# Kernel tuning notes

Hardware: AMD Instinct MI355X
Metric: run time of the kernel (lower is better)

## Reference

```python
import jax, jax.numpy as jnp
import numpy as np
from jax import lax

N_IN, N_H = 3, 2
N_REC = N_IN + N_H  # 5 qubits in the recurrent cell


def _ry(theta):
    # theta: (B,) -> (B, 2, 2) complex64 RY matrices
    c = jnp.cos(theta * 0.5).astype(jnp.complex64)
    s = jnp.sin(theta * 0.5).astype(jnp.complex64)
    return jnp.stack([jnp.stack([c, -s], -1), jnp.stack([s, c], -1)], -2)


def _rot(phi, theta, omega):
    # PennyLane Rot(phi, theta, omega) = RZ(omega) @ RY(theta) @ RZ(phi)
    c = jnp.cos(theta * 0.5)
    s = jnp.sin(theta * 0.5)
    ep = jnp.exp(-0.5j * (phi + omega))  # e^{-i(phi+omega)/2}
    em = jnp.exp(0.5j * (phi - omega))   # e^{+i(phi-omega)/2}
    m = jnp.stack([jnp.stack([ep * c, -em * s], -1),
                   jnp.stack([jnp.conj(em) * s, jnp.conj(ep) * c], -1)], -2)
    return m.astype(jnp.complex64)


def _apply1q(state, U, wire, n):
    # state: (B, 2**n); wire 0 is most significant (PennyLane convention)
    L, R = 2 ** wire, 2 ** (n - wire - 1)
    st = state.reshape(-1, L, 2, R)
    sub = 'bij,bljr->blir' if U.ndim == 3 else 'ij,bljr->blir'
    return jnp.einsum(sub, U, st).reshape(state.shape)


def _cnot_perm(c, t, n):
    # CNOT is a fixed basis permutation: flip target bit where control bit set
    cbit, tbit = 1 << (n - 1 - c), 1 << (n - 1 - t)
    idx = np.arange(2 ** n)
    return np.where(idx & cbit, idx ^ tbit, idx)


def _entangle(state, weights, n):
    # StronglyEntanglingLayers: per-wire Rot, then CNOT ring with range r
    n_layers = weights.shape[0]
    for l in range(n_layers):
        for w in range(n):
            state = _apply1q(state, _rot(weights[l, w, 0], weights[l, w, 1], weights[l, w, 2]), w, n)
        r = (l % (n - 1)) + 1
        for w in range(n):
            state = state[:, _cnot_perm(w, (w + r) % n, n)]
    return state


def _expz(state, wire, n):
    # <Z_wire> = P(0) - P(1)
    L, R = 2 ** wire, 2 ** (n - wire - 1)
    p = (state.real ** 2 + state.imag ** 2).reshape(-1, L, 2, R).sum((1, 3))
    return p[:, 0] - p[:, 1]


def _init_state(batch, n):
    s = jnp.zeros((batch, 2 ** n), jnp.complex64)
    return s.at[:, 0].set(1.0)


def _cell(x, h, w_rec):
    # batched qrnn_cell: RY-encode x on wires 0..2, h on wires 3..4, entangle, read Z(3),Z(4)
    state = _init_state(x.shape[0], N_REC)
    for i in range(N_IN):
        state = _apply1q(state, _ry(x[:, i]), i, N_REC)
    for j in range(N_H):
        state = _apply1q(state, _ry(h[:, j]), N_IN + j, N_REC)
    state = _entangle(state, w_rec, N_REC)
    return jnp.stack([_expz(state, N_IN + j, N_REC) for j in range(N_H)], -1)


def _readout(h, w_out):
    # batched qnn_readout: 2-qubit circuit, Z(0) expval
    state = _init_state(h.shape[0], N_H)
    for j in range(N_H):
        state = _apply1q(state, _ry(h[:, j]), j, N_H)
    state = _entangle(state, w_out, N_H)
    return _expz(state, 0, N_H)[:, None]


def setup_inputs() -> dict:
    key = jax.random.key(0)
    k1, k2, k3 = jax.random.split(key, 3)
    T, B = 32, 8192
    x_seq = jax.random.normal(k1, (T, B, N_IN), jnp.float32)
    w_rec = jax.random.normal(k2, (2, N_REC, 3), jnp.float32)
    w_out = jax.random.normal(k3, (2, N_H, 3), jnp.float32)
    return {"x_seq": x_seq, "w_rec": w_rec, "w_out": w_out}


def reference(x_seq, w_rec, w_out):
    B = x_seq.shape[1]

    def step(h, xt):
        return _cell(xt, h, w_rec), None

    h, _ = lax.scan(step, jnp.zeros((B, N_H), jnp.float32), x_seq)
    return _readout(h, w_out)  # (B, 1)
```

## Files before the change

### kernel.cpp

```cpp
#include <hip/hip_runtime.h>
#include <math.h>


typedef __attribute__((ext_vector_type(2))) float f2;

constexpr int cnot_ct(int idx, int c, int t) {
    return (idx & (1 << (4 - c))) ? (idx ^ (1 << (4 - t))) : idx;
}
constexpr int Pfwd_ct(int x, int r) {
    for (int w = 4; w >= 0; --w) x = cnot_ct(x, w, (w + r) % 5);
    return x;
}
constexpr int Pinv_ct(int x, int r) {
    for (int w = 0; w <= 4; ++w) x = cnot_ct(x, w, (w + r) % 5);
    return x;
}
static_assert(Pinv_ct(Pfwd_ct(13, 1), 1) == 13, "inv1");
static_assert(Pinv_ct(Pfwd_ct(22, 2), 2) == 22, "inv2");

struct PermT { int v[32]; };
constexpr PermT mkperm(int r) {
    PermT p{};
    for (int i = 0; i < 32; ++i) p.v[i] = Pfwd_ct(i, r);
    return p;
}
constexpr PermT PT1 = mkperm(1);
constexpr PermT PT2 = mkperm(2);

__device__ __forceinline__ int pinv_rt(int x, int r) {
    #pragma unroll
    for (int w = 0; w < 5; ++w) {
        int cbit = 1 << (4 - w), tbit = 1 << (4 - ((w + r) % 5));
        if (x & cbit) x ^= tbit;
    }
    return x;
}

template<int CTRL> __device__ __forceinline__ float dppf(float x) {
    return __int_as_float(__builtin_amdgcn_mov_dpp(__float_as_int(x), CTRL, 0xF, 0xF, true));
}
template<int PL> __device__ __forceinline__ float mvf(float x) {
    if constexpr (PL == 0)  return x;
    else if constexpr (PL == 1)  return dppf<0xB1>(x);
    else if constexpr (PL == 2)  return dppf<0x4E>(x);
    else if constexpr (PL == 7)  return dppf<0x141>(x);
    else if constexpr (PL == 8)  return dppf<0x128>(x);
    else { static_assert(PL == 0 || PL == 1 || PL == 2 || PL == 7 || PL == 8, "mask"); return x; }
}

template<int M>
__device__ __forceinline__ void ry_full(float (&ar)[32], float (&ai)[32],
                                        float c, float s) {
    #pragma unroll
    for (int i = 0; i < 32; ++i) {
        if (!(i & M)) {
            const int j = i | M;
            const float a0r = ar[i], a0i = ai[i], a1r = ar[j], a1i = ai[j];
            ar[i] = c * a0r - s * a1r;  ai[i] = c * a0i - s * a1i;
            ar[j] = s * a0r + c * a1r;  ai[j] = s * a0i + c * a1i;
        }
    }
}

__global__ __launch_bounds__(256, 1) void qrnn_setup(
    const float* __restrict__ w_rec, const float* __restrict__ w_out,
    float* __restrict__ ws) {

    __shared__ float CgS[10], SgS[10];
    __shared__ float P0c[32], P0s[32];
    __shared__ float E1c[32], E1s[32];
    __shared__ float RC[16];
    __shared__ float Qs[488];

    const int tid = threadIdx.x;

    if (tid < 10) {
        const float th = w_rec[(tid / 5) * 15 + (tid % 5) * 3 + 1];
        CgS[tid] = cosf(0.5f * th);
        SgS[tid] = sinf(0.5f * th);
    } else if (tid >= 32 && tid < 96) {
        const int idx = tid - 32;
        const int i = idx & 31;
        float ang = 0.f;
        if (idx < 32) {
            #pragma unroll
            for (int w = 0; w < 5; ++w)
                ang += (((i >> (4 - w)) & 1) ? 0.5f : -0.5f) * w_rec[w * 3 + 0];
            P0c[i] = cosf(ang); P0s[i] = sinf(ang);
        } else {
            const int j = pinv_rt(i, 1);
            #pragma unroll
            for (int w = 0; w < 5; ++w) {
                ang += (((i >> (4 - w)) & 1) ? 0.5f : -0.5f) * w_rec[w * 3 + 2];
                ang += (((j >> (4 - w)) & 1) ? 0.5f : -0.5f) * w_rec[15 + w * 3 + 0];
            }
            E1c[i] = cosf(ang); E1s[i] = sinf(ang);
        }
    } else if (tid >= 96 && tid < 100) {
        const int g = tid - 96;
        const int li = g >> 1, w = g & 1;
        const float phi = w_out[li * 6 + w * 3 + 0];
        const float the = w_out[li * 6 + w * 3 + 1];
        const float ome = w_out[li * 6 + w * 3 + 2];
        const float cs = cosf(0.5f * the), ss = sinf(0.5f * the);
        const float cp = cosf(0.5f * (phi + ome)), sp = sinf(0.5f * (phi + ome));
        const float cm = cosf(0.5f * (phi - ome)), sm = sinf(0.5f * (phi - ome));
        RC[g * 4 + 0] = cp * cs;
        RC[g * 4 + 1] = -sp * cs;
        RC[g * 4 + 2] = cm * ss;
        RC[g * 4 + 3] = sm * ss;
    }
    __syncthreads();

    if (tid < 243) {
        const int d0 = tid / 81, d1 = (tid / 27) % 3, d2 = (tid / 9) % 3,
                  d3 = (tid / 3) % 3, d4 = tid % 3;
        const float C3[3] = {1.f, 0.5f, 0.5f};
        const float S3[3] = {0.f, 0.86602540378443865f, -0.86602540378443865f};
        const float f0c = C3[d0], f0s = S3[d0], f1c = C3[d1], f1s = S3[d1],
                    f2c = C3[d2], f2s = S3[d2], f3c = C3[d3], f3s = S3[d3],
                    f4c = C3[d4], f4s = S3[d4];

        float ar[32], ai[32];
        #pragma unroll
        for (int i = 0; i < 32; ++i) {
            const float b = ((i & 16) ? f0s : f0c) * ((i & 8) ? f1s : f1c) *
                            ((i & 4) ? f2s : f2c) * ((i & 2) ? f3s : f3c) *
                            ((i & 1) ? f4s : f4c);
            ar[i] = b * P0c[i]; ai[i] = b * P0s[i];
        }
        ry_full<16>(ar, ai, CgS[0], SgS[0]);
        ry_full<8>(ar, ai, CgS[1], SgS[1]);
        ry_full<4>(ar, ai, CgS[2], SgS[2]);
        ry_full<2>(ar, ai, CgS[3], SgS[3]);
        ry_full<1>(ar, ai, CgS[4], SgS[4]);
        #pragma unroll
        for (int i = 0; i < 32; ++i) {
            const float nr = ar[i] * E1c[i] - ai[i] * E1s[i];
            const float ni = ar[i] * E1s[i] + ai[i] * E1c[i];
            ar[i] = nr; ai[i] = ni;
        }
        float br[32], bi[32];
        #pragma unroll
        for (int i = 0; i < 32; ++i) { br[i] = ar[PT1.v[i]]; bi[i] = ai[PT1.v[i]]; }
        ry_full<16>(br, bi, CgS[5], SgS[5]);
        ry_full<8>(br, bi, CgS[6], SgS[6]);
        ry_full<4>(br, bi, CgS[7], SgS[7]);
        ry_full<2>(br, bi, CgS[8], SgS[8]);
        ry_full<1>(br, bi, CgS[9], SgS[9]);
        float q0 = 0.f, q1 = 0.f;
        #pragma unroll
        for (int i = 0; i < 32; ++i) {
            const int src = PT2.v[i];
            const float p = br[src] * br[src] + bi[src] * bi[src];
            q0 += ((i >> 1) & 1) ? -p : p;
            q1 += (i & 1) ? -p : p;
        }
        Qs[tid * 2 + 0] = q0; Qs[tid * 2 + 1] = q1;
    }
    __syncthreads();

    const float W[3][3] = {{1.f/3.f, 1.f/3.f, 1.f/3.f},
                           {2.f/3.f, -1.f/3.f, -1.f/3.f},
                           {0.f, 0.57735026918962576f, -0.57735026918962576f}};
    for (int o = tid; o < 486; o += 256) {
        const int row = o / 27, col = o % 27;
        const int j = row / 9, pq = row % 9, p = pq / 3, q = pq % 3;
        const int a0 = col / 9, a1 = (col / 3) % 3, a2 = col % 3;
        float acc = 0.f;
        for (int dd0 = 0; dd0 < 3; ++dd0)
        for (int dd1 = 0; dd1 < 3; ++dd1)
        for (int dd2 = 0; dd2 < 3; ++dd2) {
            const float w012 = W[a0][dd0] * W[a1][dd1] * W[a2][dd2];
            for (int dd3 = 0; dd3 < 3; ++dd3)
            for (int dd4 = 0; dd4 < 3; ++dd4) {
                const int c = (((dd0 * 3 + dd1) * 3 + dd2) * 3 + dd3) * 3 + dd4;
                acc = fmaf(w012 * W[p][dd3] * W[q][dd4], Qs[c * 2 + j], acc);
            }
        }
        ws[row * 28 + col] = acc;
    }
    if (tid < 18) ws[tid * 28 + 27] = 0.f;
    if (tid < 16) ws[18 * 28 + tid] = RC[tid];
}

__global__ __launch_bounds__(256, 3) void qrnn_run(
    const float* __restrict__ x_seq, const float* __restrict__ A_g,
    float* __restrict__ out, int B) {

    __shared__ __align__(16) float4 xs4[16 * 33];
    __shared__ float Cm[16][19][33];

    const int tloc = threadIdx.x;
    const int grp  = tloc >> 4;
    const int k    = tloc & 15;
    const int b0   = blockIdx.x * 16;
    const int b    = b0 + grp;

    #pragma unroll
    for (int qq = 0; qq < 2; ++qq) {
        const int p = tloc + qq * 256;
        const int ts = p >> 4, lbs = p & 15;
        const int gidx = (ts * B + (b0 + lbs)) * 3;
        float4 v;
        v.x = x_seq[gidx]; v.y = x_seq[gidx + 1]; v.z = x_seq[gidx + 2]; v.w = 0.f;
        xs4[lbs * 33 + ts] = v;
    }
    __syncthreads();

    constexpr float Kf = 0.15915494309189535f;
    float Xb0[28], Xb1[28];
    #pragma unroll
    for (int tt = 0; tt < 2; ++tt) {
        float* Xb = tt ? Xb1 : Xb0;
        const float4 xv = xs4[grp * 33 + k + 16 * tt];
        const float cx0 = __builtin_amdgcn_cosf(xv.x * Kf);
        const float sx0 = __builtin_amdgcn_cosf(fmaf(xv.x, Kf, -0.25f));
        const float cx1 = __builtin_amdgcn_cosf(xv.y * Kf);
        const float sx1 = __builtin_amdgcn_cosf(fmaf(xv.y, Kf, -0.25f));
        const float cx2 = __builtin_amdgcn_cosf(xv.z * Kf);
        const float sx2 = __builtin_amdgcn_cosf(fmaf(xv.z, Kf, -0.25f));
        Xb[0] = 1.f;  Xb[1] = cx2;       Xb[2] = sx2;
        Xb[3] = cx1;  Xb[4] = cx1 * cx2; Xb[5] = cx1 * sx2;
        Xb[6] = sx1;  Xb[7] = sx1 * cx2; Xb[8] = sx1 * sx2;
        #pragma unroll
        for (int i = 0; i < 9; ++i) { Xb[9 + i] = cx0 * Xb[i]; Xb[18 + i] = sx0 * Xb[i]; }
        Xb[27] = 0.f;
    }
    {
        const float4* A4p = (const float4*)A_g;
        #pragma unroll 1
        for (int r = 0; r < 18; ++r) {
            float4 av[7];
            #pragma unroll
            for (int i = 0; i < 7; ++i) av[i] = A4p[r * 7 + i];
            float a00 = 0.f, a01 = 0.f, a10 = 0.f, a11 = 0.f;
            #pragma unroll
            for (int i = 0; i < 7; ++i) {
                a00 = fmaf(av[i].x, Xb0[4*i+0], a00); a00 = fmaf(av[i].y, Xb0[4*i+1], a00);
                a01 = fmaf(av[i].z, Xb0[4*i+2], a01); a01 = fmaf(av[i].w, Xb0[4*i+3], a01);
                a10 = fmaf(av[i].x, Xb1[4*i+0], a10); a10 = fmaf(av[i].y, Xb1[4*i+1], a10);
                a11 = fmaf(av[i].z, Xb1[4*i+2], a11); a11 = fmaf(av[i].w, Xb1[4*i+3], a11);
            }
            Cm[grp][r][k]      = a00 + a01;
            Cm[grp][r][k + 16] = a10 + a11;
        }
        Cm[grp][18][k] = 0.f; Cm[grp][18][k + 16] = 0.f;
    }

    const int jj = k >> 3;
    const int term = (k & 7) + 1;
    const int rowA = jj * 9 + term;
    const int rowB = (k == 0) ? 0 : ((k == 8) ? 9 : 18);
    const int p = term / 3, q = term % 3;
    const float* CA_ptr = &Cm[grp][rowA][0];
    const float* CB_ptr = &Cm[grp][rowB][0];

    float h0 = 0.f, h1 = 0.f;
    float CA = CA_ptr[0], CB = CB_ptr[0];
    #pragma unroll 1
    for (int t = 0; t < 32; ++t) {
        const int tn = (t < 31) ? t + 1 : 31;
        const float CAn = CA_ptr[tn], CBn = CB_ptr[tn];
        const float ch0 = __builtin_amdgcn_cosf(h0 * Kf);
        const float sh0 = __builtin_amdgcn_cosf(fmaf(h0, Kf, -0.25f));
        const float ch1 = __builtin_amdgcn_cosf(h1 * Kf);
        const float sh1 = __builtin_amdgcn_cosf(fmaf(h1, Kf, -0.25f));
        const float u = (p == 1) ? ch0 : ((p == 2) ? sh0 : 1.f);
        const float v = (q == 1) ? ch1 : ((q == 2) ? sh1 : 1.f);
        float val = fmaf(CA, u * v, CB);
        val += mvf<1>(val);
        val += mvf<2>(val);
        val += mvf<7>(val);
        const float other = mvf<8>(val);
        h0 = (k & 8) ? other : val;
        h1 = (k & 8) ? val : other;
        CA = CAn; CB = CBn;
    }

    float rc[16];
    {
        const float4* RCp = (const float4*)(A_g + 18 * 28);
        #pragma unroll
        for (int i = 0; i < 4; ++i) {
            const float4 v = RCp[i];
            rc[4*i+0] = v.x; rc[4*i+1] = v.y; rc[4*i+2] = v.z; rc[4*i+3] = v.w;
        }
    }
    constexpr float K2 = 0.5f * 0.15915494309189535f;
    const float ch0 = __builtin_amdgcn_cosf(h0 * K2);
    const float sh0 = __builtin_amdgcn_cosf(fmaf(h0, K2, -0.25f));
    const float ch1 = __builtin_amdgcn_cosf(h1 * K2);
    const float sh1 = __builtin_amdgcn_cosf(fmaf(h1, K2, -0.25f));
    float vr0 = ch0 * ch1, vr1 = ch0 * sh1, vr2 = sh0 * ch1, vr3 = sh0 * sh1;
    float vi0 = 0.f, vi1 = 0.f, vi2 = 0.f, vi3 = 0.f;

    #pragma unroll
    for (int li = 0; li < 2; ++li) {
        #pragma unroll
        for (int w = 0; w < 2; ++w) {
            const int g = li * 2 + w;
            const float are = rc[g*4+0], aim = rc[g*4+1];
            const float bre = rc[g*4+2], bim = rc[g*4+3];
            #define AP2(r0, i0, r1, i1) do {                                  \
                float n0r = are*(r0) - aim*(i0) - bre*(r1) + bim*(i1);        \
                float n0i = are*(i0) + aim*(r0) - bre*(i1) - bim*(r1);        \
                float n1r = bre*(r0) + bim*(i0) + are*(r1) + aim*(i1);        \
                float n1i = bre*(i0) - bim*(r0) + are*(i1) - aim*(r1);        \
                r0 = n0r; i0 = n0i; r1 = n1r; i1 = n1i; } while (0)
            if (w == 0) { AP2(vr0, vi0, vr2, vi2); AP2(vr1, vi1, vr3, vi3); }
            else        { AP2(vr0, vi0, vr1, vi1); AP2(vr2, vi2, vr3, vi3); }
            #undef AP2
        }
        float tr1 = vr2, ti1 = vi2, tr2 = vr3, ti2 = vi3, tr3 = vr1, ti3 = vi1;
        vr1 = tr1; vi1 = ti1; vr2 = tr2; vi2 = ti2; vr3 = tr3; vi3 = ti3;
    }

    const float outv = (vr0 * vr0 + vi0 * vi0 + vr1 * vr1 + vi1 * vi1) -
                       (vr2 * vr2 + vi2 * vi2 + vr3 * vr3 + vi3 * vi3);
    if (k == 0) out[b] = outv;
}

extern "C" void kernel_launch(void* const* d_in, const int* in_sizes, int n_in,
                              void* d_out, int out_size, void* d_ws, size_t ws_size,
                              hipStream_t stream) {
    const float* x_seq = (const float*)d_in[0];
    const float* w_rec = (const float*)d_in[1];
    const float* w_out = (const float*)d_in[2];
    float* out = (float*)d_out;
    float* ws  = (float*)d_ws;

    const int B = out_size;
    const int grid = (B * 16) / 256;

    hipLaunchKernelGGL(qrnn_setup, dim3(1), dim3(256), 0, stream, w_rec, w_out, ws);
    hipLaunchKernelGGL(qrnn_run, dim3(grid), dim3(256), 0, stream,
                       x_seq, ws, out, B);
}
```

Baseline: 77.88 us.

## Fuse weight-setup kernel into main recurrent kernel, recomputing coefficient tables per block

The single-block setup kernel is merged into the main kernel, so every block rebuilds the 18x28 coefficient table in shared memory instead of reading it from a workspace written by a separate launch. This removes one launch and the serial dependency on a one-block kernel. To keep the per-block setup cheap, the 243-way contraction is split into two separable stages, and the CNOT permutations are folded into gate and sign masks rather than applied as register copies. The cost is redundant setup work in all 512 blocks, plus shared memory reused between the setup scratch and the per-batch tables. A register double-buffer is also added for the A-row loads.

```diff
diff --git a/kernel.cpp b/kernel.cpp
--- a/kernel.cpp
+++ b/kernel.cpp
@@ -1,8 +1,6 @@
 #include <hip/hip_runtime.h>
 #include <math.h>
 
-
-typedef __attribute__((ext_vector_type(2))) float f2;
 
 constexpr int cnot_ct(int idx, int c, int t) {
     return (idx & (1 << (4 - c))) ? (idx ^ (1 << (4 - t))) : idx;
@@ -18,14 +16,40 @@
 static_assert(Pinv_ct(Pfwd_ct(13, 1), 1) == 13, "inv1");
 static_assert(Pinv_ct(Pfwd_ct(22, 2), 2) == 22, "inv2");
 
-struct PermT { int v[32]; };
-constexpr PermT mkperm(int r) {
-    PermT p{};
-    for (int i = 0; i < 32; ++i) p.v[i] = Pfwd_ct(i, r);
-    return p;
-}
-constexpr PermT PT1 = mkperm(1);
-constexpr PermT PT2 = mkperm(2);
+constexpr int GMASK[10] = {16, 8, 4, 2, 1,
+                           Pfwd_ct(16,1), Pfwd_ct(8,1), Pfwd_ct(4,1), Pfwd_ct(2,1), Pfwd_ct(1,1)};
+constexpr int fmask_l1(int pb) {
+    int f = 0;
+    for (int b = 0; b < 5; ++b) if ((Pinv_ct(1 << b, 1) >> pb) & 1) f |= 1 << b;
+    return f;
+}
+constexpr int FMASK[10] = {16, 8, 4, 2, 1,
+                           fmask_l1(4), fmask_l1(3), fmask_l1(2), fmask_l1(1), fmask_l1(0)};
+constexpr int cinv_ct(int x) { return Pinv_ct(Pinv_ct(x, 1), 2); }
+constexpr int fmask_fin(int pb) {
+    int f = 0;
+    for (int b = 0; b < 5; ++b) if ((cinv_ct(1 << b) >> pb) & 1) f |= 1 << b;
+    return f;
+}
+constexpr int SF3 = fmask_fin(1);
+constexpr int SF4 = fmask_fin(0);
+
+constexpr bool gates_straddle() {
+    for (int g = 0; g < 10; ++g)
+        if (!(__builtin_popcount(GMASK[g] & FMASK[g]) & 1)) return false;
+    return true;
+}
+static_assert(gates_straddle(), "GMASK/FMASK straddle");
+
+constexpr unsigned span3_ct(int a, int b, int c) {
+    unsigned m = 0;
+    for (int i = 0; i < 8; ++i) {
+        int v = ((i & 1) ? a : 0) ^ ((i & 2) ? b : 0) ^ ((i & 4) ? c : 0);
+        m |= 1u << v;
+    }
+    return m;
+}
+static_assert(span3_ct(1, 2, 7) == 0xFFu, "butterfly {1,2,7} spans lanes 0..7");
 
 __device__ __forceinline__ int pinv_rt(int x, int r) {
     #pragma unroll
@@ -40,46 +64,63 @@
     return __int_as_float(__builtin_amdgcn_mov_dpp(__float_as_int(x), CTRL, 0xF, 0xF, true));
 }
 template<int PL> __device__ __forceinline__ float mvf(float x) {
-    if constexpr (PL == 0)  return x;
-    else if constexpr (PL == 1)  return dppf<0xB1>(x);
-    else if constexpr (PL == 2)  return dppf<0x4E>(x);
-    else if constexpr (PL == 7)  return dppf<0x141>(x);
-    else if constexpr (PL == 8)  return dppf<0x128>(x);
-    else { static_assert(PL == 0 || PL == 1 || PL == 2 || PL == 7 || PL == 8, "mask"); return x; }
-}
-
-template<int M>
-__device__ __forceinline__ void ry_full(float (&ar)[32], float (&ai)[32],
-                                        float c, float s) {
+    if constexpr (PL == 1)      return dppf<0xB1>(x);
+    else if constexpr (PL == 2) return dppf<0x4E>(x);
+    else if constexpr (PL == 7) return dppf<0x141>(x);
+    else if constexpr (PL == 8) return dppf<0x128>(x);
+    else { static_assert(PL == 1 || PL == 2 || PL == 7 || PL == 8, "mask"); return x; }
+}
+
+template<int g>
+__device__ __forceinline__ void gate_full(float (&ar)[32], float (&ai)[32],
+                                          float c, float s) {
+    constexpr int m = GMASK[g], F = FMASK[g];
     #pragma unroll
     for (int i = 0; i < 32; ++i) {
-        if (!(i & M)) {
-            const int j = i | M;
-            const float a0r = ar[i], a0i = ai[i], a1r = ar[j], a1i = ai[j];
-            ar[i] = c * a0r - s * a1r;  ai[i] = c * a0i - s * a1i;
-            ar[j] = s * a0r + c * a1r;  ai[j] = s * a0i + c * a1i;
-        }
-    }
-}
-
-__global__ __launch_bounds__(256, 1) void qrnn_setup(
-    const float* __restrict__ w_rec, const float* __restrict__ w_out,
-    float* __restrict__ ws) {
-
+        if ((__builtin_popcount(i & F) & 1) == 0) {
+            const int j = i ^ m;
+            const float r0 = ar[i], i0 = ai[i], r1 = ar[j], i1 = ai[j];
+            ar[i] = c * r0 - s * r1;  ai[i] = c * i0 - s * i1;
+            ar[j] = s * r0 + c * r1;  ai[j] = s * i0 + c * i1;
+        }
+    }
+}
+
+__global__ __launch_bounds__(256, 3) void qrnn_fused(
+    const float* __restrict__ x_seq, const float* __restrict__ w_rec,
+    const float* __restrict__ w_out, float* __restrict__ out, int B) {
+
+    __shared__ __align__(16) float4 xs4[16 * 33];
+    __shared__ __align__(16) float A2s[18 * 28];
     __shared__ float CgS[10], SgS[10];
-    __shared__ float P0c[32], P0s[32];
-    __shared__ float E1c[32], E1s[32];
+    __shared__ float P0c[32], P0s[32], E1c[32], E1s[32];
     __shared__ float RC[16];
-    __shared__ float Qs[488];
-
-    const int tid = threadIdx.x;
-
-    if (tid < 10) {
-        const float th = w_rec[(tid / 5) * 15 + (tid % 5) * 3 + 1];
-        CgS[tid] = cosf(0.5f * th);
-        SgS[tid] = sinf(0.5f * th);
-    } else if (tid >= 32 && tid < 96) {
-        const int idx = tid - 32;
+    __shared__ __align__(16) float Cm_pool[16 * 19 * 33];
+    float* const Qs  = Cm_pool;
+    float* const P1s = Cm_pool + 512;
+
+    const int tloc = threadIdx.x;
+    const int grp  = tloc >> 4;
+    const int k    = tloc & 15;
+    const int b0   = blockIdx.x * 16;
+    const int b    = b0 + grp;
+
+    #pragma unroll
+    for (int qq = 0; qq < 2; ++qq) {
+        const int p = tloc + qq * 256;
+        const int ts = p >> 4, lbs = p & 15;
+        const int gidx = (ts * B + (b0 + lbs)) * 3;
+        float4 v;
+        v.x = x_seq[gidx]; v.y = x_seq[gidx + 1]; v.z = x_seq[gidx + 2]; v.w = 0.f;
+        xs4[lbs * 33 + ts] = v;
+    }
+
+    if (tloc < 10) {
+        const float th = w_rec[(tloc / 5) * 15 + (tloc % 5) * 3 + 1];
+        CgS[tloc] = cosf(0.5f * th);
+        SgS[tloc] = sinf(0.5f * th);
+    } else if (tloc >= 32 && tloc < 96) {
+        const int idx = tloc - 32;
         const int i = idx & 31;
         float ang = 0.f;
         if (idx < 32) {
@@ -96,8 +137,8 @@
             }
             E1c[i] = cosf(ang); E1s[i] = sinf(ang);
         }
-    } else if (tid >= 96 && tid < 100) {
-        const int g = tid - 96;
+    } else if (tloc >= 96 && tloc < 100) {
+        const int g = tloc - 96;
         const int li = g >> 1, w = g & 1;
         const float phi = w_out[li * 6 + w * 3 + 0];
         const float the = w_out[li * 6 + w * 3 + 1];
@@ -112,9 +153,9 @@
     }
     __syncthreads();
 
-    if (tid < 243) {
-        const int d0 = tid / 81, d1 = (tid / 27) % 3, d2 = (tid / 9) % 3,
-                  d3 = (tid / 3) % 3, d4 = tid % 3;
+    if (tloc < 243) {
+        const int d0 = tloc / 81, d1 = (tloc / 27) % 3, d2 = (tloc / 9) % 3,
+                  d3 = (tloc / 3) % 3, d4 = tloc % 3;
         const float C3[3] = {1.f, 0.5f, 0.5f};
         const float S3[3] = {0.f, 0.86602540378443865f, -0.86602540378443865f};
         const float f0c = C3[d0], f0s = S3[d0], f1c = C3[d1], f1s = S3[d1],
@@ -124,88 +165,76 @@
         float ar[32], ai[32];
         #pragma unroll
         for (int i = 0; i < 32; ++i) {
-            const float b = ((i & 16) ? f0s : f0c) * ((i & 8) ? f1s : f1c) *
-                            ((i & 4) ? f2s : f2c) * ((i & 2) ? f3s : f3c) *
-                            ((i & 1) ? f4s : f4c);
-            ar[i] = b * P0c[i]; ai[i] = b * P0s[i];
-        }
-        ry_full<16>(ar, ai, CgS[0], SgS[0]);
-        ry_full<8>(ar, ai, CgS[1], SgS[1]);
-        ry_full<4>(ar, ai, CgS[2], SgS[2]);
-        ry_full<2>(ar, ai, CgS[3], SgS[3]);
-        ry_full<1>(ar, ai, CgS[4], SgS[4]);
+            const float bb = ((i & 16) ? f0s : f0c) * ((i & 8) ? f1s : f1c) *
+                             ((i & 4) ? f2s : f2c) * ((i & 2) ? f3s : f3c) *
+                             ((i & 1) ? f4s : f4c);
+            ar[i] = bb * P0c[i]; ai[i] = bb * P0s[i];
+        }
+        gate_full<0>(ar, ai, CgS[0], SgS[0]);
+        gate_full<1>(ar, ai, CgS[1], SgS[1]);
+        gate_full<2>(ar, ai, CgS[2], SgS[2]);
+        gate_full<3>(ar, ai, CgS[3], SgS[3]);
+        gate_full<4>(ar, ai, CgS[4], SgS[4]);
         #pragma unroll
         for (int i = 0; i < 32; ++i) {
             const float nr = ar[i] * E1c[i] - ai[i] * E1s[i];
             const float ni = ar[i] * E1s[i] + ai[i] * E1c[i];
             ar[i] = nr; ai[i] = ni;
         }
-        float br[32], bi[32];
-        #pragma unroll
-        for (int i = 0; i < 32; ++i) { br[i] = ar[PT1.v[i]]; bi[i] = ai[PT1.v[i]]; }
-        ry_full<16>(br, bi, CgS[5], SgS[5]);
-        ry_full<8>(br, bi, CgS[6], SgS[6]);
-        ry_full<4>(br, bi, CgS[7], SgS[7]);
-        ry_full<2>(br, bi, CgS[8], SgS[8]);
-        ry_full<1>(br, bi, CgS[9], SgS[9]);
+        gate_full<5>(ar, ai, CgS[5], SgS[5]);
+        gate_full<6>(ar, ai, CgS[6], SgS[6]);
+        gate_full<7>(ar, ai, CgS[7], SgS[7]);
+        gate_full<8>(ar, ai, CgS[8], SgS[8]);
+        gate_full<9>(ar, ai, CgS[9], SgS[9]);
         float q0 = 0.f, q1 = 0.f;
         #pragma unroll
         for (int i = 0; i < 32; ++i) {
-            const int src = PT2.v[i];
-            const float p = br[src] * br[src] + bi[src] * bi[src];
-            q0 += ((i >> 1) & 1) ? -p : p;
-            q1 += (i & 1) ? -p : p;
-        }
-        Qs[tid * 2 + 0] = q0; Qs[tid * 2 + 1] = q1;
+            const float p = ar[i] * ar[i] + ai[i] * ai[i];
+            q0 += (__builtin_popcount(i & SF3) & 1) ? -p : p;
+            q1 += (__builtin_popcount(i & SF4) & 1) ? -p : p;
+        }
+        Qs[tloc * 2 + 0] = q0; Qs[tloc * 2 + 1] = q1;
     }
     __syncthreads();
 
     const float W[3][3] = {{1.f/3.f, 1.f/3.f, 1.f/3.f},
                            {2.f/3.f, -1.f/3.f, -1.f/3.f},
                            {0.f, 0.57735026918962576f, -0.57735026918962576f}};
-    for (int o = tid; o < 486; o += 256) {
+    for (int o = tloc; o < 486; o += 256) {
+        const int j = o & 1, e = o >> 1;
+        const int d012 = e / 9, pq = e % 9, p = pq / 3, q = pq % 3;
+        float acc = 0.f;
+        #pragma unroll
+        for (int d3 = 0; d3 < 3; ++d3) {
+            const float wp = W[p][d3];
+            #pragma unroll
+            for (int d4 = 0; d4 < 3; ++d4)
+                acc = fmaf(wp * W[q][d4], Qs[(d012 * 9 + d3 * 3 + d4) * 2 + j], acc);
+        }
+        P1s[(d012 * 9 + pq) * 2 + j] = acc;
+    }
+    __syncthreads();
+
+    for (int o = tloc; o < 486; o += 256) {
         const int row = o / 27, col = o % 27;
-        const int j = row / 9, pq = row % 9, p = pq / 3, q = pq % 3;
+        const int j = row / 9, pq = row % 9;
         const int a0 = col / 9, a1 = (col / 3) % 3, a2 = col % 3;
         float acc = 0.f;
-        for (int dd0 = 0; dd0 < 3; ++dd0)
-        for (int dd1 = 0; dd1 < 3; ++dd1)
-        for (int dd2 = 0; dd2 < 3; ++dd2) {
-            const float w012 = W[a0][dd0] * W[a1][dd1] * W[a2][dd2];
-            for (int dd3 = 0; dd3 < 3; ++dd3)
-            for (int dd4 = 0; dd4 < 3; ++dd4) {
-                const int c = (((dd0 * 3 + dd1) * 3 + dd2) * 3 + dd3) * 3 + dd4;
-                acc = fmaf(w012 * W[p][dd3] * W[q][dd4], Qs[c * 2 + j], acc);
+        #pragma unroll
+        for (int dd0 = 0; dd0 < 3; ++dd0) {
+            const float w0 = W[a0][dd0];
+            #pragma unroll
+            for (int dd1 = 0; dd1 < 3; ++dd1) {
+                const float w01 = w0 * W[a1][dd1];
+                #pragma unroll
+                for (int dd2 = 0; dd2 < 3; ++dd2)
+                    acc = fmaf(w01 * W[a2][dd2],
+                               P1s[((dd0 * 9 + dd1 * 3 + dd2) * 9 + pq) * 2 + j], acc);
             }
         }
-        ws[row * 28 + col] = acc;
-    }
-    if (tid < 18) ws[tid * 28 + 27] = 0.f;
-    if (tid < 16) ws[18 * 28 + tid] = RC[tid];
-}
-
-__global__ __launch_bounds__(256, 3) void qrnn_run(
-    const float* __restrict__ x_seq, const float* __restrict__ A_g,
-    float* __restrict__ out, int B) {
-
-    __shared__ __align__(16) float4 xs4[16 * 33];
-    __shared__ float Cm[16][19][33];
-
-    const int tloc = threadIdx.x;
-    const int grp  = tloc >> 4;
-    const int k    = tloc & 15;
-    const int b0   = blockIdx.x * 16;
-    const int b    = b0 + grp;
-
-    #pragma unroll
-    for (int qq = 0; qq < 2; ++qq) {
-        const int p = tloc + qq * 256;
-        const int ts = p >> 4, lbs = p & 15;
-        const int gidx = (ts * B + (b0 + lbs)) * 3;
-        float4 v;
-        v.x = x_seq[gidx]; v.y = x_seq[gidx + 1]; v.z = x_seq[gidx + 2]; v.w = 0.f;
-        xs4[lbs * 33 + ts] = v;
-    }
+        A2s[row * 28 + col] = acc;
+    }
+    if (tloc < 18) A2s[tloc * 28 + 27] = 0.f;
     __syncthreads();
 
     constexpr float Kf = 0.15915494309189535f;
@@ -228,12 +257,17 @@
         Xb[27] = 0.f;
     }
     {
-        const float4* A4p = (const float4*)A_g;
+        const float4* Ap = (const float4*)A2s;
+        float* const Cmg = Cm_pool + grp * (19 * 33);
+        float4 av[7], nv[7];
+        #pragma unroll
+        for (int i = 0; i < 7; ++i) av[i] = Ap[i];
         #pragma unroll 1
         for (int r = 0; r < 18; ++r) {
-            float4 av[7];
-            #pragma unroll
-            for (int i = 0; i < 7; ++i) av[i] = A4p[r * 7 + i];
+            if (r < 17) {
+                #pragma unroll
+                for (int i = 0; i < 7; ++i) nv[i] = Ap[(r + 1) * 7 + i];
+            }
             float a00 = 0.f, a01 = 0.f, a10 = 0.f, a11 = 0.f;
             #pragma unroll
             for (int i = 0; i < 7; ++i) {
@@ -242,10 +276,12 @@
                 a10 = fmaf(av[i].x, Xb1[4*i+0], a10); a10 = fmaf(av[i].y, Xb1[4*i+1], a10);
                 a11 = fmaf(av[i].z, Xb1[4*i+2], a11); a11 = fmaf(av[i].w, Xb1[4*i+3], a11);
             }
-            Cm[grp][r][k]      = a00 + a01;
-            Cm[grp][r][k + 16] = a10 + a11;
-        }
-        Cm[grp][18][k] = 0.f; Cm[grp][18][k + 16] = 0.f;
+            Cmg[r * 33 + k]      = a00 + a01;
+            Cmg[r * 33 + k + 16] = a10 + a11;
+            #pragma unroll
+            for (int i = 0; i < 7; ++i) av[i] = nv[i];
+        }
+        Cmg[18 * 33 + k] = 0.f; Cmg[18 * 33 + k + 16] = 0.f;
     }
 
     const int jj = k >> 3;
@@ -253,8 +289,8 @@
     const int rowA = jj * 9 + term;
     const int rowB = (k == 0) ? 0 : ((k == 8) ? 9 : 18);
     const int p = term / 3, q = term % 3;
-    const float* CA_ptr = &Cm[grp][rowA][0];
-    const float* CB_ptr = &Cm[grp][rowB][0];
+    const float* CA_ptr = Cm_pool + grp * (19 * 33) + rowA * 33;
+    const float* CB_ptr = Cm_pool + grp * (19 * 33) + rowB * 33;
 
     float h0 = 0.f, h1 = 0.f;
     float CA = CA_ptr[0], CB = CB_ptr[0];
@@ -278,15 +314,6 @@
         CA = CAn; CB = CBn;
     }
 
-    float rc[16];
-    {
-        const float4* RCp = (const float4*)(A_g + 18 * 28);
-        #pragma unroll
-        for (int i = 0; i < 4; ++i) {
-            const float4 v = RCp[i];
-            rc[4*i+0] = v.x; rc[4*i+1] = v.y; rc[4*i+2] = v.z; rc[4*i+3] = v.w;
-        }
-    }
     constexpr float K2 = 0.5f * 0.15915494309189535f;
     const float ch0 = __builtin_amdgcn_cosf(h0 * K2);
     const float sh0 = __builtin_amdgcn_cosf(fmaf(h0, K2, -0.25f));
@@ -300,8 +327,8 @@
         #pragma unroll
         for (int w = 0; w < 2; ++w) {
             const int g = li * 2 + w;
-            const float are = rc[g*4+0], aim = rc[g*4+1];
-            const float bre = rc[g*4+2], bim = rc[g*4+3];
+            const float are = RC[g*4+0], aim = RC[g*4+1];
+            const float bre = RC[g*4+2], bim = RC[g*4+3];
             #define AP2(r0, i0, r1, i1) do {                                  \
                 float n0r = are*(r0) - aim*(i0) - bre*(r1) + bim*(i1);        \
                 float n0i = are*(i0) + aim*(r0) - bre*(i1) - bim*(r1);        \
@@ -328,12 +355,10 @@
     const float* w_rec = (const float*)d_in[1];
     const float* w_out = (const float*)d_in[2];
     float* out = (float*)d_out;
-    float* ws  = (float*)d_ws;
 
     const int B = out_size;
     const int grid = (B * 16) / 256;
 
-    hipLaunchKernelGGL(qrnn_setup, dim3(1), dim3(256), 0, stream, w_rec, w_out, ws);
-    hipLaunchKernelGGL(qrnn_run, dim3(grid), dim3(256), 0, stream,
-                       x_seq, ws, out, B);
-}
+    hipLaunchKernelGGL(qrnn_fused, dim3(grid), dim3(256), 0, stream,
+                       x_seq, w_rec, w_out, out, B);
+}
```

New measurement: 76.31 us. -2.0%, faster.
